# Performance work log

Hardware: AMD Instinct MI355X
Metric: run time of the kernel (lower is better)

## Reference

```python
import jax, jax.numpy as jnp
import numpy as np

ALPHA = 0.5  # args.alpha (restart probability in feature propagation)


def _knn_adj(x, k):
    # pairwise squared euclidean distances (cdist^2), self-distance masked out
    n = x.shape[0]
    sq = jnp.sum(x * x, axis=1)
    d = sq[:, None] + sq[None, :] - 2.0 * (x @ x.T)          # [N, N]
    d = d + jnp.eye(n, dtype=x.dtype) * 1e30                  # exclude self
    _, idx = jax.lax.top_k(-d, k)                              # [N, k] nearest neighbors
    # row-normalized knn adjacency with 1/k weights
    rows = jnp.arange(n)[:, None]
    return jnp.zeros((n, n), x.dtype).at[rows, idx].set(1.0 / k)


def _propagate(adj, x, l, alpha):
    # h_{t+1} = (1-alpha) * A h_t + alpha * x, for l hops
    h = x
    for _ in range(l):
        h = (1.0 - alpha) * (adj @ h) + alpha * x
    return h


def setup_inputs() -> dict:
    key = jax.random.key(0)
    ks = jax.random.split(key, 8)
    N, NFEAT, NHID = 10000, 128, 64
    x = jax.random.normal(ks[0], (N, NFEAT), dtype=jnp.float32)
    adj = jax.random.uniform(ks[1], (N, N), dtype=jnp.float32)
    adj = adj / jnp.sum(adj, axis=1, keepdims=True)            # row-normalized operator
    s_e = 1.0 / np.sqrt(NFEAT)
    s_h = 1.0 / np.sqrt(NHID)
    s_d = 1.0 / np.sqrt(2 * NHID)
    return {
        "x": x,
        "adj": adj,
        "W_enc": jax.random.normal(ks[2], (NFEAT, NHID), jnp.float32) * s_e,
        "b_enc": jnp.zeros((NHID,), jnp.float32),
        "W_enc2": jax.random.normal(ks[3], (NHID, NHID), jnp.float32) * s_h,
        "b_enc2": jnp.zeros((NHID,), jnp.float32),
        "W_dec": jax.random.normal(ks[4], (2 * NHID, NFEAT), jnp.float32) * s_d,
        "b_dec": jnp.zeros((NFEAT,), jnp.float32),
        "k": 16,
        "l": 5,
    }


def reference(x, adj, W_enc, b_enc, W_enc2, b_enc2, W_dec, b_dec, k, l):
    knn = _knn_adj(x, k)                                       # get_knn_graph(x, args.k)
    h1 = _propagate(adj, x, l, ALPHA)                          # feature_propagation(adj, ...)
    h1 = jax.nn.relu(h1 @ W_enc + b_enc)                       # encoder (dropout inactive at eval)
    h2 = _propagate(knn, x, l, ALPHA)                          # feature_propagation(knn, ...)
    h2 = jax.nn.relu(h2 @ W_enc + b_enc)
    z1 = jax.nn.relu(h1 @ W_enc2 + b_enc2)                     # encoder_2
    z2 = jax.nn.relu(h2 @ W_enc2 + b_enc2)
    h = jnp.concatenate([z1, z2], axis=1)                      # [N, 2*nhid]
    res = h @ W_dec + b_dec                                    # decoder
    return (h1, h2, res @ res.T)
```

## Files before the change

kernel.cpp:

```cpp
#include <hip/hip_runtime.h>
#include <stdint.h>


typedef unsigned short u16;
typedef unsigned int u32;
typedef unsigned char u8;

#define N_NODES 10000
#define NPAD    10112
#define KPAD    10240
#define JPAD    10240
#define NF      128
#define NH      64
#define CAP     96
#define ADJ_SCALE 4096.0f
#define ADJ_INV   (0.5f / 4096.0f)

using short8 = __attribute__((ext_vector_type(8))) short;
using f32x4  = __attribute__((ext_vector_type(4))) float;

__device__ __forceinline__ u16 f2bf(float f) {
  u32 u = __float_as_uint(f);
  u += 0x7FFFu + ((u >> 16) & 1u);
  return (u16)(u >> 16);
}
__device__ __forceinline__ float bf2f(u16 h) { return __uint_as_float(((u32)h) << 16); }

__device__ __forceinline__ u32 pk4_fp8(float a, float b, float c, float d) {
  int v = __builtin_amdgcn_cvt_pk_fp8_f32(a, b, 0, false);
  v = __builtin_amdgcn_cvt_pk_fp8_f32(c, d, v, true);
  return (u32)v;
}

__device__ __forceinline__ void g2lds16(const void* g, void* l) {
  __builtin_amdgcn_global_load_lds((const __attribute__((address_space(1))) void*)g,
                                   (__attribute__((address_space(3))) void*)l, 16, 0, 0);
}


__global__ __launch_bounds__(256) void k_rowops(const float* __restrict__ x,
    u16* __restrict__ xhi, u16* __restrict__ xlo, float* __restrict__ sq) {
  int w = threadIdx.x >> 6, lane = threadIdx.x & 63;
  int row = blockIdx.x * 4 + w;
  if (row >= JPAD) return;
  int f = lane * 2;
  if (row < N_NODES) {
    float2 v = *(const float2*)(x + (size_t)row * NF + f);
    u16 h0 = f2bf(v.x), h1 = f2bf(v.y);
    float l0 = v.x - bf2f(h0), l1 = v.y - bf2f(h1);
    u16 e0 = f2bf(l0), e1 = f2bf(l1);
    *(u32*)(xhi + (size_t)row * NF + f) = (u32)h0 | ((u32)h1 << 16);
    *(u32*)(xlo + (size_t)row * NF + f) = (u32)e0 | ((u32)e1 << 16);
    float s = v.x * v.x + v.y * v.y;
#pragma unroll
    for (int o = 32; o > 0; o >>= 1) s += __shfl_xor(s, o);
    if (lane == 0) sq[row] = s;
  } else {
    *(u32*)(xhi + (size_t)row * NF + f) = 0u;
    *(u32*)(xlo + (size_t)row * NF + f) = 0u;
    if (lane == 0) sq[row] = 1.0e30f;
  }
}

__global__ __launch_bounds__(256) void k_transpose(const float* __restrict__ x,
    float* __restrict__ xTf, float* __restrict__ hTf) {
  __shared__ float tile[32][33];
  int k0 = blockIdx.x * 32, f0 = blockIdx.y * 32;
  int c = threadIdx.x & 31, r4 = threadIdx.x >> 5;
#pragma unroll
  for (int i = 0; i < 4; i++) {
    int r = r4 + i * 8;
    int k = k0 + r;
    float v = 0.f;
    if (k < N_NODES) v = x[(size_t)k * NF + f0 + c];
    tile[r][c] = v;
  }
  __syncthreads();
#pragma unroll
  for (int i = 0; i < 4; i++) {
    int r = r4 + i * 8;
    int f = f0 + r;
    int k = k0 + c;
    float v = tile[c][r];
    size_t idx = (size_t)f * KPAD + k;
    xTf[idx] = v; hTf[idx] = v;
  }
}

__global__ __launch_bounds__(256) void k_pack8(const float* __restrict__ hTf,
                                               u8* __restrict__ hT8) {
  int idx = (blockIdx.x * 256 + threadIdx.x) * 4;
  float4 v = *(const float4*)(hTf + idx);
  *(u32*)(hT8 + idx) = pk4_fp8(v.x, v.y, v.z, v.w);
}

__global__ __launch_bounds__(256) void k_adjcvt(const float* __restrict__ adj,
                                                u8* __restrict__ out) {
  const int UNITS = NPAD * (KPAD / 8);
  for (int u = blockIdx.x * 256 + threadIdx.x; u < UNITS; u += gridDim.x * 256) {
    int r = u / (KPAD / 8);
    int c = (u - r * (KPAD / 8)) * 8;
    float v[8];
    if (r < N_NODES && c + 7 < N_NODES) {
      const float* p = adj + (size_t)r * N_NODES + c;
      float4 a = *(const float4*)p;
      float4 b = *(const float4*)(p + 4);
      v[0]=a.x; v[1]=a.y; v[2]=a.z; v[3]=a.w;
      v[4]=b.x; v[5]=b.y; v[6]=b.z; v[7]=b.w;
    } else {
#pragma unroll
      for (int t = 0; t < 8; t++) {
        int cc = c + t;
        v[t] = (r < N_NODES && cc < N_NODES) ? adj[(size_t)r * N_NODES + cc] : 0.f;
      }
    }
#pragma unroll
    for (int t = 0; t < 8; t++) v[t] *= ADJ_SCALE;
    uint2 pk;
    pk.x = pk4_fp8(v[0], v[1], v[2], v[3]);
    pk.y = pk4_fp8(v[4], v[5], v[6], v[7]);
    *(uint2*)(out + (size_t)r * KPAD + c) = pk;
  }
}


__global__ __launch_bounds__(256) void k_gram(const u16* __restrict__ xhi,
    const u16* __restrict__ xlo, const float* __restrict__ sqg,
    float2* __restrict__ cand, u32* __restrict__ cnts) {
  __shared__ __align__(16) u16 shi[64 * 128];
  __shared__ __align__(16) u16 slo[64 * 128];
  __shared__ __align__(16) float ssq[64];
  const int tid = threadIdx.x, w = tid >> 6, lane = tid & 63;
  const int l15 = lane & 15, g = lane >> 4;
  const int q = blockIdx.x * 64 + w * 16 + l15;
  const int split = blockIdx.y;
  const size_t cbase = ((size_t)q * 16 + split * 4 + g) * CAP;

  short8 bh[4], bl[4];
#pragma unroll
  for (int ks = 0; ks < 4; ks++) {
    size_t off = (size_t)q * NF + ks * 32 + g * 8;
    bh[ks] = *(const short8*)(xhi + off);
    bl[ks] = *(const short8*)(xlo + off);
  }
  float t4[4] = {3.0e38f, 3.0e38f, 3.0e38f, 3.0e38f};
  float thr = 3.0e38f;
  u32 cnt = 0;

  for (int ch = 0; ch < 40; ch++) {
    int jbase = split * 2560 + ch * 64;
    __syncthreads();
#pragma unroll
    for (int r = 0; r < 4; r++) {
      int s = r * 256 + tid;
      int row = s >> 4, u = s & 15;
      int uu = u ^ (row & 7);
      size_t goff = (size_t)(jbase + row) * NF + uu * 8;
      g2lds16(xhi + goff, (void*)(shi + ((s & ~63) << 3)));
      g2lds16(xlo + goff, (void*)(slo + ((s & ~63) << 3)));
    }
    if (tid < 64) ssq[tid] = sqg[jbase + tid];
    __syncthreads();

#pragma unroll
    for (int sub = 0; sub < 4; sub++) {
      f32x4 acc = {0.f, 0.f, 0.f, 0.f};
#pragma unroll
      for (int ks = 0; ks < 4; ks++) {
        int row = sub * 16 + l15;
        int uu = ((ks * 4 + g) ^ (row & 7));
        int idx = row * 128 + uu * 8;
        short8 ah = *(const short8*)(shi + idx);
        short8 al = *(const short8*)(slo + idx);
        acc = __builtin_amdgcn_mfma_f32_16x16x32_bf16(ah, bh[ks], acc, 0, 0, 0);
        acc = __builtin_amdgcn_mfma_f32_16x16x32_bf16(ah, bl[ks], acc, 0, 0, 0);
        acc = __builtin_amdgcn_mfma_f32_16x16x32_bf16(al, bh[ks], acc, 0, 0, 0);
      }
      f32x4 sv = *(const f32x4*)(ssq + sub * 16 + g * 4);
      int jb = jbase + sub * 16 + g * 4;
#pragma unroll
      for (int reg = 0; reg < 4; reg++) {
        int j = jb + reg;
        float dd = sv[reg] - 2.0f * acc[reg];
        dd = (j == q) ? 3.0e38f : dd;
        if (dd < thr) {
          if (cnt < CAP) cand[cbase + cnt] = make_float2(dd, __int_as_float(j));
          cnt++;
        }
        bool c0 = dd < t4[0], c1 = dd < t4[1], c2 = dd < t4[2], c3 = dd < t4[3];
        t4[3] = c2 ? t4[2] : (c3 ? dd : t4[3]);
        t4[2] = c1 ? t4[1] : (c2 ? dd : t4[2]);
        t4[1] = c0 ? t4[0] : (c1 ? dd : t4[1]);
        t4[0] = c0 ? dd : t4[0];
      }
      float m = t4[3];
      m = fminf(m, 3.0e38f);
      m = fmaxf(m, __shfl_xor(m, 16));
      m = fmaxf(m, __shfl_xor(m, 32));
      thr = m;
    }
  }
  cnts[(size_t)q * 16 + split * 4 + g] = (cnt < CAP) ? cnt : CAP;
}

__global__ __launch_bounds__(256) void k_merge(const float2* __restrict__ cand,
    const u32* __restrict__ cnts, int* __restrict__ knn) {
  int w = threadIdx.x >> 6, lane = threadIdx.x & 63;
  int q = blockIdx.x * 4 + w;
  if (q >= N_NODES) return;
  int r = lane >> 2, s = lane & 3;
  int cnt = (int)cnts[(size_t)q * 16 + r];
  const float2* cv = cand + ((size_t)q * 16 + r) * CAP;

  float t[16]; int ti[16];
#pragma unroll
  for (int i = 0; i < 16; i++) { t[i] = 3.0e38f; ti[i] = -1; }
  for (int e = s; e < cnt; e += 4) {
    float2 v = cv[e];
    float dd = v.x; int j = __float_as_int(v.y);
    if (j == q) continue;
    if (dd < t[15]) {
#pragma unroll
      for (int i = 15; i >= 1; --i) {
        bool ltp = dd < t[i - 1];
        bool ltc = dd < t[i];
        t[i]  = ltp ? t[i - 1] : (ltc ? dd : t[i]);
        ti[i] = ltp ? ti[i - 1] : (ltc ? j : ti[i]);
      }
      if (dd < t[0]) { t[0] = dd; ti[0] = j; }
    }
  }
  int myout = -1;
#pragma unroll
  for (int round = 0; round < 16; round++) {
    float d0 = t[0]; int j0 = ti[0];
#pragma unroll
    for (int off = 32; off > 0; off >>= 1) {
      float dn = __shfl_xor(d0, off); int jn = __shfl_xor(j0, off);
      bool take = (dn < d0) || (dn == d0 && jn < j0);
      d0 = take ? dn : d0; j0 = take ? jn : j0;
    }
    if (ti[0] == j0) {
#pragma unroll
      for (int i = 0; i < 15; i++) { t[i] = t[i + 1]; ti[i] = ti[i + 1]; }
      t[15] = 3.0e38f; ti[15] = -1;
    }
    if (lane == round) myout = j0;
  }
  if (lane < 16) knn[q * 16 + lane] = myout;
}

__global__ __launch_bounds__(256) void k_knnprop(const float* __restrict__ src,
    const float* __restrict__ x, const int* __restrict__ knn, float* __restrict__ dst) {
  int w = threadIdx.x >> 6, lane = threadIdx.x & 63;
  int row = blockIdx.x * 4 + w;
  if (row >= N_NODES) return;
  int f = lane * 2;
  float a0 = 0.f, a1 = 0.f;
#pragma unroll
  for (int nb = 0; nb < 16; nb++) {
    int j = knn[row * 16 + nb];
    float2 v = *(const float2*)(src + (size_t)j * NF + f);
    a0 += v.x; a1 += v.y;
  }
  float2 xv = *(const float2*)(x + (size_t)row * NF + f);
  float2 o;
  o.x = a0 * (0.5f / 16.f) + 0.5f * xv.x;
  o.y = a1 * (0.5f / 16.f) + 0.5f * xv.y;
  *(float2*)(dst + (size_t)row * NF + f) = o;
}


__global__ __launch_bounds__(256) void k_gemm(const u8* __restrict__ adj8,
    const u8* __restrict__ hT8, float* __restrict__ parts) {
  __shared__ __align__(16) u8 As[128 * 64];
  __shared__ __align__(16) u8 Bs[128 * 64];
  const int tid = threadIdx.x, w = tid >> 6, lane = tid & 63;
  const int l15 = lane & 15, g = lane >> 4;
  const int m0 = blockIdx.x * 128;
  const int split = blockIdx.y;
  const int wm = (w & 1) * 64, wn = (w >> 1) * 64;

  f32x4 zero = {0.f, 0.f, 0.f, 0.f};
  f32x4 acc[4][4];
#pragma unroll
  for (int mi = 0; mi < 4; mi++)
#pragma unroll
    for (int ni = 0; ni < 4; ni++) acc[mi][ni] = zero;

  for (int it = 0; it < 20; it++) {
    int kk = split * 1280 + it * 64;
    __syncthreads();
#pragma unroll
    for (int r = 0; r < 2; r++) {
      int s = r * 256 + tid;
      int row = s >> 2, u = s & 3;
      int uu = u ^ ((row >> 1) & 3);
      g2lds16(adj8 + (size_t)(m0 + row) * KPAD + kk + uu * 16, (void*)(As + ((s & ~63) << 4)));
    }
#pragma unroll
    for (int r = 0; r < 2; r++) {
      int s = r * 256 + tid;
      int row = s >> 2, u = s & 3;
      int uu = u ^ ((row >> 1) & 3);
      g2lds16(hT8 + (size_t)row * KPAD + kk + uu * 16, (void*)(Bs + ((s & ~63) << 4)));
    }
    __syncthreads();
#pragma unroll
    for (int ks = 0; ks < 2; ks++) {
      long af[4], bf[4];
#pragma unroll
      for (int mi = 0; mi < 4; mi++) {
        int row = wm + mi * 16 + l15;
        int u = (ks * 2 + (g >> 1)) ^ ((row >> 1) & 3);
        af[mi] = *(const long*)(As + row * 64 + u * 16 + (g & 1) * 8);
      }
#pragma unroll
      for (int ni = 0; ni < 4; ni++) {
        int row = wn + ni * 16 + l15;
        int u = (ks * 2 + (g >> 1)) ^ ((row >> 1) & 3);
        bf[ni] = *(const long*)(Bs + row * 64 + u * 16 + (g & 1) * 8);
      }
#pragma unroll
      for (int mi = 0; mi < 4; mi++)
#pragma unroll
        for (int ni = 0; ni < 4; ni++)
          acc[mi][ni] = __builtin_amdgcn_mfma_f32_16x16x32_fp8_fp8(af[mi], bf[ni], acc[mi][ni], 0, 0, 0);
    }
  }
#pragma unroll
  for (int mi = 0; mi < 4; mi++) {
#pragma unroll
    for (int ni = 0; ni < 4; ni++) {
      int n = wn + ni * 16 + l15;
      int m = m0 + wm + mi * 16 + g * 4;
      *(f32x4*)(parts + (size_t)(split * 128 + n) * NPAD + m) = acc[mi][ni];
    }
  }
}

__global__ __launch_bounds__(256) void k_reduce(const float* __restrict__ parts,
    const float* __restrict__ xTf, float* __restrict__ hTf, u8* __restrict__ hT8) {
  int idx = (blockIdx.x * 256 + threadIdx.x) * 4;
  int n = idx / KPAD;
  int k = idx - n * KPAD;
  float4 h = {0.f, 0.f, 0.f, 0.f};
  if (k < NPAD) {
    float4 s = {0.f, 0.f, 0.f, 0.f};
#pragma unroll
    for (int sp = 0; sp < 8; sp++) {
      float4 v = *(const float4*)(parts + (size_t)(sp * 128 + n) * NPAD + k);
      s.x += v.x; s.y += v.y; s.z += v.z; s.w += v.w;
    }
    float4 xv = *(const float4*)(xTf + (size_t)n * KPAD + k);
    h.x = ADJ_INV * s.x + 0.5f * xv.x;
    h.y = ADJ_INV * s.y + 0.5f * xv.y;
    h.z = ADJ_INV * s.z + 0.5f * xv.z;
    h.w = ADJ_INV * s.w + 0.5f * xv.w;
  }
  *(float4*)(hTf + (size_t)n * KPAD + k) = h;
  *(u32*)(hT8 + (size_t)n * KPAD + k) = pk4_fp8(h.x, h.y, h.z, h.w);
}


__global__ __launch_bounds__(256) void k_enc(const float* __restrict__ src, int sf, int si,
    const float* __restrict__ W, const float* __restrict__ b, float* __restrict__ out) {
  int w = threadIdx.x >> 6, o = threadIdx.x & 63;
  int row = blockIdx.x * 4 + w;
  if (row >= N_NODES) return;
  float acc = b[o];
#pragma unroll 8
  for (int f = 0; f < NF; f++) {
    float hv = src[(size_t)f * sf + (size_t)row * si];
    acc += hv * W[f * NH + o];
  }
  out[(size_t)row * NH + o] = fmaxf(acc, 0.f);
}

__global__ __launch_bounds__(256) void k_zres(const float* __restrict__ h1e,
    const float* __restrict__ h2e, const float* __restrict__ W2, const float* __restrict__ b2,
    const float* __restrict__ Wd, const float* __restrict__ bd, u16* __restrict__ resb) {
  int w = threadIdx.x >> 6, o = threadIdx.x & 63;
  int row = blockIdx.x * 4 + w;
  if (row >= NPAD) return;
  if (row >= N_NODES) {
    *(u32*)(resb + (size_t)row * NF + o * 2) = 0u;
    return;
  }
  float z1 = b2[o], z2 = b2[o];
#pragma unroll 8
  for (int c = 0; c < NH; c++) {
    float wv = W2[c * NH + o];
    z1 += h1e[(size_t)row * NH + c] * wv;
    z2 += h2e[(size_t)row * NH + c] * wv;
  }
  z1 = fmaxf(z1, 0.f); z2 = fmaxf(z2, 0.f);
  float r0 = bd[o], r1 = bd[o + 64];
#pragma unroll 4
  for (int c = 0; c < NH; c++) {
    float v1 = __shfl(z1, c), v2 = __shfl(z2, c);
    r0 += v1 * Wd[c * NF + o]      + v2 * Wd[(c + 64) * NF + o];
    r1 += v1 * Wd[c * NF + o + 64] + v2 * Wd[(c + 64) * NF + o + 64];
  }
  resb[(size_t)row * NF + o] = f2bf(r0);
  resb[(size_t)row * NF + o + 64] = f2bf(r1);
}


__global__ __launch_bounds__(256) void k_out2(const u16* __restrict__ resb,
                                              float* __restrict__ out2) {
  const int tid = threadIdx.x, w = tid >> 6, lane = tid & 63;
  const int l15 = lane & 15, g = lane >> 4;
  const int m0 = blockIdx.x * 128 + (w & 1) * 64;
  const int n0 = blockIdx.y * 128 + (w >> 1) * 64;
  short8 af[4][4];
#pragma unroll
  for (int mi = 0; mi < 4; mi++)
#pragma unroll
    for (int ks = 0; ks < 4; ks++)
      af[mi][ks] = *(const short8*)(resb + (size_t)(m0 + mi * 16 + l15) * NF + ks * 32 + g * 8);
  f32x4 acc[4][4];
#pragma unroll
  for (int ni = 0; ni < 4; ni++) {
    short8 bq[4];
#pragma unroll
    for (int ks = 0; ks < 4; ks++)
      bq[ks] = *(const short8*)(resb + (size_t)(n0 + ni * 16 + l15) * NF + ks * 32 + g * 8);
#pragma unroll
    for (int mi = 0; mi < 4; mi++) {
      f32x4 a = {0.f, 0.f, 0.f, 0.f};
#pragma unroll
      for (int ks = 0; ks < 4; ks++)
        a = __builtin_amdgcn_mfma_f32_16x16x32_bf16(af[mi][ks], bq[ks], a, 0, 0, 0);
      acc[mi][ni] = a;
    }
  }
#pragma unroll
  for (int mi = 0; mi < 4; mi++) {
#pragma unroll
    for (int ni = 0; ni < 4; ni++) {
      int n = n0 + ni * 16 + l15;
      int mb = m0 + mi * 16 + g * 4;
      if (n < N_NODES) {
#pragma unroll
        for (int reg = 0; reg < 4; reg++) {
          int m = mb + reg;
          if (m < N_NODES) out2[(size_t)m * N_NODES + n] = acc[mi][ni][reg];
        }
      }
    }
  }
}


extern "C" void kernel_launch(void* const* d_in, const int* in_sizes, int n_in,
                              void* d_out, int out_size, void* d_ws, size_t ws_size,
                              hipStream_t stream) {
  (void)in_sizes; (void)n_in; (void)out_size; (void)ws_size;
  const float* x     = (const float*)d_in[0];
  const float* adj   = (const float*)d_in[1];
  const float* Wenc  = (const float*)d_in[2];
  const float* benc  = (const float*)d_in[3];
  const float* Wenc2 = (const float*)d_in[4];
  const float* benc2 = (const float*)d_in[5];
  const float* Wdec  = (const float*)d_in[6];
  const float* bdec  = (const float*)d_in[7];

  char* ws = (char*)d_ws;
  size_t off = 0;
  auto alloc = [&](size_t bytes) {
    void* p = ws + off;
    off = (off + bytes + 255) & ~(size_t)255;
    return p;
  };
  u8*     adj8 = (u8*)    alloc((size_t)NPAD * KPAD);
  void*   uni  =          alloc((size_t)10240 * 16 * CAP * 8);
  float*  hTf  = (float*) alloc((size_t)128 * KPAD * 4);
  u8*     hT8  = (u8*)    alloc((size_t)128 * KPAD);
  float*  xTf  = (float*) alloc((size_t)128 * KPAD * 4);
  u16*    xhi  = (u16*)   alloc((size_t)JPAD * NF * 2);
  u16*    xlo  = (u16*)   alloc((size_t)JPAD * NF * 2);
  float*  sq   = (float*) alloc((size_t)JPAD * 4);
  u32*    cnts = (u32*)   alloc((size_t)10240 * 16 * 4);
  int*    knn  = (int*)   alloc((size_t)N_NODES * 16 * 4);
  float*  h2a  = (float*) alloc((size_t)N_NODES * NF * 4);
  float*  h2b  = (float*) alloc((size_t)N_NODES * NF * 4);
  u16*    resb = (u16*)   alloc((size_t)NPAD * NF * 2);

  float2* cand = (float2*)uni;
  float*  parts= (float*) uni;

  float* out0 = (float*)d_out;
  float* out1 = out0 + 640000;
  float* out2 = out0 + 1280000;

  k_rowops   <<<dim3(JPAD / 4), dim3(256), 0, stream>>>(x, xhi, xlo, sq);
  k_transpose<<<dim3(KPAD / 32, 4), dim3(256), 0, stream>>>(x, xTf, hTf);
  k_pack8    <<<dim3(1280), dim3(256), 0, stream>>>(hTf, hT8);
  k_adjcvt   <<<dim3(8192), dim3(256), 0, stream>>>(adj, adj8);

  k_gram <<<dim3(158, 4), dim3(256), 0, stream>>>(xhi, xlo, sq, cand, cnts);
  k_merge<<<dim3(2500), dim3(256), 0, stream>>>(cand, cnts, knn);

  const float* h2s = x; float* h2d = h2a; float* h2o = h2b;
  for (int t = 0; t < 5; t++) {
    k_knnprop<<<dim3(2500), dim3(256), 0, stream>>>(h2s, x, knn, h2d);
    h2s = h2d; float* tmp = h2d; h2d = h2o; h2o = tmp;
  }

  for (int t = 0; t < 5; t++) {
    k_gemm  <<<dim3(79, 8), dim3(256), 0, stream>>>(adj8, hT8, parts);
    k_reduce<<<dim3(1280), dim3(256), 0, stream>>>(parts, xTf, hTf, hT8);
  }

  k_enc<<<dim3(2500), dim3(256), 0, stream>>>(hTf, KPAD, 1, Wenc, benc, out0);
  k_enc<<<dim3(2500), dim3(256), 0, stream>>>((const float*)h2s, 1, NF, Wenc, benc, out1);
  k_zres<<<dim3(2528), dim3(256), 0, stream>>>(out0, out1, Wenc2, benc2, Wdec, bdec, resb);
  k_out2<<<dim3(79, 79), dim3(256), 0, stream>>>(resb, out2);
}
```

Before: 1.332 ms.

## Fuse independent stages into heterogeneous launches and store GEMM partials as bf16

Independent stages now share a single launch by splitting block ranges: setup combines row ops, transpose and fp8 packing; gram runs alongside adj conversion; the adj GEMM runs alongside the knn merge or knn propagation; the reduce runs alongside knn propagation. The encoder and head kernels are folded into one. GEMM split-K partials are stored as bf16 rather than fp32, and the gram top-k update is skipped when no lane has a candidate. This cuts launch count and lets small bandwidth-bound work fill gaps beside the compute-heavy kernels, at the cost of reduced-precision partial sums and larger combined kernels.

```diff
diff --git a/kernel.cpp b/kernel.cpp
--- a/kernel.cpp
+++ b/kernel.cpp
@@ -16,8 +16,16 @@
 #define ADJ_SCALE 4096.0f
 #define ADJ_INV   (0.5f / 4096.0f)
 
+#define GRAM_BLKS  632
+#define ADJ_BLKS   1024
+#define GEMM_BLKS  632
+#define MERGE_BLKS 2500
+#define RED_BLKS   1280
+#define KNNP_BLKS  2500
+
 using short8 = __attribute__((ext_vector_type(8))) short;
 using f32x4  = __attribute__((ext_vector_type(4))) float;
+using u16x4  = __attribute__((ext_vector_type(4))) unsigned short;
 
 __device__ __forceinline__ u16 f2bf(float f) {
   u32 u = __float_as_uint(f);
@@ -38,66 +46,142 @@
 }
 
 
-__global__ __launch_bounds__(256) void k_rowops(const float* __restrict__ x,
-    u16* __restrict__ xhi, u16* __restrict__ xlo, float* __restrict__ sq) {
-  int w = threadIdx.x >> 6, lane = threadIdx.x & 63;
-  int row = blockIdx.x * 4 + w;
-  if (row >= JPAD) return;
-  int f = lane * 2;
-  if (row < N_NODES) {
-    float2 v = *(const float2*)(x + (size_t)row * NF + f);
-    u16 h0 = f2bf(v.x), h1 = f2bf(v.y);
-    float l0 = v.x - bf2f(h0), l1 = v.y - bf2f(h1);
-    u16 e0 = f2bf(l0), e1 = f2bf(l1);
-    *(u32*)(xhi + (size_t)row * NF + f) = (u32)h0 | ((u32)h1 << 16);
-    *(u32*)(xlo + (size_t)row * NF + f) = (u32)e0 | ((u32)e1 << 16);
-    float s = v.x * v.x + v.y * v.y;
-#pragma unroll
-    for (int o = 32; o > 0; o >>= 1) s += __shfl_xor(s, o);
-    if (lane == 0) sq[row] = s;
+__global__ __launch_bounds__(256) void k_setup(const float* __restrict__ x,
+    u16* __restrict__ xhi, u16* __restrict__ xlo, float* __restrict__ sq,
+    float* __restrict__ xTf, float* __restrict__ hTf, u8* __restrict__ hT8) {
+  __shared__ float tile[32][33];
+  int bid = blockIdx.x;
+  if (bid < 2560) {
+    int w = threadIdx.x >> 6, lane = threadIdx.x & 63;
+    int row = bid * 4 + w;
+    if (row >= JPAD) return;
+    int f = lane * 2;
+    if (row < N_NODES) {
+      float2 v = *(const float2*)(x + (size_t)row * NF + f);
+      u16 h0 = f2bf(v.x), h1 = f2bf(v.y);
+      float l0 = v.x - bf2f(h0), l1 = v.y - bf2f(h1);
+      u16 e0 = f2bf(l0), e1 = f2bf(l1);
+      *(u32*)(xhi + (size_t)row * NF + f) = (u32)h0 | ((u32)h1 << 16);
+      *(u32*)(xlo + (size_t)row * NF + f) = (u32)e0 | ((u32)e1 << 16);
+      float s = v.x * v.x + v.y * v.y;
+#pragma unroll
+      for (int o = 32; o > 0; o >>= 1) s += __shfl_xor(s, o);
+      if (lane == 0) sq[row] = s;
+    } else {
+      *(u32*)(xhi + (size_t)row * NF + f) = 0u;
+      *(u32*)(xlo + (size_t)row * NF + f) = 0u;
+      if (lane == 0) sq[row] = 1.0e30f;
+    }
   } else {
-    *(u32*)(xhi + (size_t)row * NF + f) = 0u;
-    *(u32*)(xlo + (size_t)row * NF + f) = 0u;
-    if (lane == 0) sq[row] = 1.0e30f;
-  }
-}
-
-__global__ __launch_bounds__(256) void k_transpose(const float* __restrict__ x,
-    float* __restrict__ xTf, float* __restrict__ hTf) {
-  __shared__ float tile[32][33];
-  int k0 = blockIdx.x * 32, f0 = blockIdx.y * 32;
-  int c = threadIdx.x & 31, r4 = threadIdx.x >> 5;
-#pragma unroll
-  for (int i = 0; i < 4; i++) {
-    int r = r4 + i * 8;
-    int k = k0 + r;
-    float v = 0.f;
-    if (k < N_NODES) v = x[(size_t)k * NF + f0 + c];
-    tile[r][c] = v;
-  }
-  __syncthreads();
-#pragma unroll
-  for (int i = 0; i < 4; i++) {
-    int r = r4 + i * 8;
-    int f = f0 + r;
-    int k = k0 + c;
-    float v = tile[c][r];
-    size_t idx = (size_t)f * KPAD + k;
-    xTf[idx] = v; hTf[idx] = v;
-  }
-}
-
-__global__ __launch_bounds__(256) void k_pack8(const float* __restrict__ hTf,
-                                               u8* __restrict__ hT8) {
-  int idx = (blockIdx.x * 256 + threadIdx.x) * 4;
-  float4 v = *(const float4*)(hTf + idx);
-  *(u32*)(hT8 + idx) = pk4_fp8(v.x, v.y, v.z, v.w);
-}
-
-__global__ __launch_bounds__(256) void k_adjcvt(const float* __restrict__ adj,
-                                                u8* __restrict__ out) {
+    int id2 = bid - 2560;
+    int k0 = (id2 % 320) * 32, f0 = (id2 / 320) * 32;
+    int c = threadIdx.x & 31, r4 = threadIdx.x >> 5;
+#pragma unroll
+    for (int i = 0; i < 4; i++) {
+      int r = r4 + i * 8;
+      int k = k0 + r;
+      float v = 0.f;
+      if (k < N_NODES) v = x[(size_t)k * NF + f0 + c];
+      tile[r][c] = v;
+    }
+    __syncthreads();
+#pragma unroll
+    for (int i = 0; i < 4; i++) {
+      int r = r4 + i * 8;
+      int f = f0 + r;
+      int k = k0 + c;
+      float v = tile[c][r];
+      size_t idx = (size_t)f * KPAD + k;
+      xTf[idx] = v; hTf[idx] = v;
+      hT8[idx] = (u8)(__builtin_amdgcn_cvt_pk_fp8_f32(v, 0.f, 0, false) & 0xff);
+    }
+  }
+}
+
+
+__device__ __forceinline__ void dev_gram(int bx, int split,
+    u16* shi, u16* slo, float* ssq,
+    const u16* __restrict__ xhi, const u16* __restrict__ xlo,
+    const float* __restrict__ sqg, float2* __restrict__ cand, u32* __restrict__ cnts) {
+  const int tid = threadIdx.x, w = tid >> 6, lane = tid & 63;
+  const int l15 = lane & 15, g = lane >> 4;
+  const int q = bx * 64 + w * 16 + l15;
+  const size_t cbase = ((size_t)q * 16 + split * 4 + g) * CAP;
+
+  short8 bh[4], bl[4];
+#pragma unroll
+  for (int ks = 0; ks < 4; ks++) {
+    size_t off = (size_t)q * NF + ks * 32 + g * 8;
+    bh[ks] = *(const short8*)(xhi + off);
+    bl[ks] = *(const short8*)(xlo + off);
+  }
+  float t4[4] = {3.0e38f, 3.0e38f, 3.0e38f, 3.0e38f};
+  float thr = 3.0e38f;
+  u32 cnt = 0;
+
+  for (int ch = 0; ch < 40; ch++) {
+    int jbase = split * 2560 + ch * 64;
+    __syncthreads();
+#pragma unroll
+    for (int r = 0; r < 4; r++) {
+      int s = r * 256 + tid;
+      int row = s >> 4, u = s & 15;
+      int uu = u ^ (row & 7);
+      size_t goff = (size_t)(jbase + row) * NF + uu * 8;
+      g2lds16(xhi + goff, (void*)(shi + ((s & ~63) << 3)));
+      g2lds16(xlo + goff, (void*)(slo + ((s & ~63) << 3)));
+    }
+    if (tid < 64) ssq[tid] = sqg[jbase + tid];
+    __syncthreads();
+
+#pragma unroll
+    for (int sub = 0; sub < 4; sub++) {
+      f32x4 acc = {0.f, 0.f, 0.f, 0.f};
+#pragma unroll
+      for (int ks = 0; ks < 4; ks++) {
+        int row = sub * 16 + l15;
+        int uu = ((ks * 4 + g) ^ (row & 7));
+        int idx = row * 128 + uu * 8;
+        short8 ah = *(const short8*)(shi + idx);
+        short8 al = *(const short8*)(slo + idx);
+        acc = __builtin_amdgcn_mfma_f32_16x16x32_bf16(ah, bh[ks], acc, 0, 0, 0);
+        acc = __builtin_amdgcn_mfma_f32_16x16x32_bf16(ah, bl[ks], acc, 0, 0, 0);
+        acc = __builtin_amdgcn_mfma_f32_16x16x32_bf16(al, bh[ks], acc, 0, 0, 0);
+      }
+      f32x4 sv = *(const f32x4*)(ssq + sub * 16 + g * 4);
+      int jb = jbase + sub * 16 + g * 4;
+#pragma unroll
+      for (int reg = 0; reg < 4; reg++) {
+        int j = jb + reg;
+        float dd = sv[reg] - 2.0f * acc[reg];
+        dd = (j == q) ? 3.0e38f : dd;
+        if (__any(dd < thr)) {
+          if (dd < thr) {
+            if (cnt < CAP) cand[cbase + cnt] = make_float2(dd, __int_as_float(j));
+            cnt++;
+          }
+          bool c0 = dd < t4[0], c1 = dd < t4[1], c2 = dd < t4[2], c3 = dd < t4[3];
+          t4[3] = c2 ? t4[2] : (c3 ? dd : t4[3]);
+          t4[2] = c1 ? t4[1] : (c2 ? dd : t4[2]);
+          t4[1] = c0 ? t4[0] : (c1 ? dd : t4[1]);
+          t4[0] = c0 ? dd : t4[0];
+        }
+      }
+      float m = t4[3];
+      m = fminf(m, 3.0e38f);
+      m = fmaxf(m, __shfl_xor(m, 16));
+      m = fmaxf(m, __shfl_xor(m, 32));
+      thr = m;
+    }
+  }
+  cnts[(size_t)q * 16 + split * 4 + g] = (cnt < CAP) ? cnt : CAP;
+}
+
+
+__device__ __forceinline__ void dev_adjcvt(int rb, const float* __restrict__ adj,
+                                           u8* __restrict__ out) {
   const int UNITS = NPAD * (KPAD / 8);
-  for (int u = blockIdx.x * 256 + threadIdx.x; u < UNITS; u += gridDim.x * 256) {
+  for (int u = rb * 256 + (int)threadIdx.x; u < UNITS; u += ADJ_BLKS * 256) {
     int r = u / (KPAD / 8);
     int c = (u - r * (KPAD / 8)) * 8;
     float v[8];
@@ -124,89 +208,94 @@
 }
 
 
-__global__ __launch_bounds__(256) void k_gram(const u16* __restrict__ xhi,
+__global__ __launch_bounds__(256) void k_gram_adj(const u16* __restrict__ xhi,
     const u16* __restrict__ xlo, const float* __restrict__ sqg,
-    float2* __restrict__ cand, u32* __restrict__ cnts) {
-  __shared__ __align__(16) u16 shi[64 * 128];
-  __shared__ __align__(16) u16 slo[64 * 128];
-  __shared__ __align__(16) float ssq[64];
+    float2* __restrict__ cand, u32* __restrict__ cnts,
+    const float* __restrict__ adj, u8* __restrict__ adj8) {
+  __shared__ __align__(16) u8 smem[33024];
+  int bid = blockIdx.x;
+  if (bid < GRAM_BLKS) {
+    dev_gram(bid % 158, bid / 158, (u16*)smem, (u16*)(smem + 16384),
+             (float*)(smem + 32768), xhi, xlo, sqg, cand, cnts);
+  } else {
+    dev_adjcvt(bid - GRAM_BLKS, adj, adj8);
+  }
+}
+
+
+__device__ __forceinline__ void dev_gemm(int rid, u8* As, u8* Bs,
+    const u8* __restrict__ adj8, const u8* __restrict__ hT8, u16* __restrict__ parts16) {
   const int tid = threadIdx.x, w = tid >> 6, lane = tid & 63;
   const int l15 = lane & 15, g = lane >> 4;
-  const int q = blockIdx.x * 64 + w * 16 + l15;
-  const int split = blockIdx.y;
-  const size_t cbase = ((size_t)q * 16 + split * 4 + g) * CAP;
-
-  short8 bh[4], bl[4];
-#pragma unroll
-  for (int ks = 0; ks < 4; ks++) {
-    size_t off = (size_t)q * NF + ks * 32 + g * 8;
-    bh[ks] = *(const short8*)(xhi + off);
-    bl[ks] = *(const short8*)(xlo + off);
-  }
-  float t4[4] = {3.0e38f, 3.0e38f, 3.0e38f, 3.0e38f};
-  float thr = 3.0e38f;
-  u32 cnt = 0;
-
-  for (int ch = 0; ch < 40; ch++) {
-    int jbase = split * 2560 + ch * 64;
+  const int m0 = (rid % 79) * 128;
+  const int split = rid / 79;
+  const int wm = (w & 1) * 64, wn = (w >> 1) * 64;
+
+  f32x4 zero = {0.f, 0.f, 0.f, 0.f};
+  f32x4 acc[4][4];
+#pragma unroll
+  for (int mi = 0; mi < 4; mi++)
+#pragma unroll
+    for (int ni = 0; ni < 4; ni++) acc[mi][ni] = zero;
+
+  for (int it = 0; it < 20; it++) {
+    int kk = split * 1280 + it * 64;
     __syncthreads();
 #pragma unroll
-    for (int r = 0; r < 4; r++) {
+    for (int r = 0; r < 2; r++) {
       int s = r * 256 + tid;
-      int row = s >> 4, u = s & 15;
-      int uu = u ^ (row & 7);
-      size_t goff = (size_t)(jbase + row) * NF + uu * 8;
-      g2lds16(xhi + goff, (void*)(shi + ((s & ~63) << 3)));
-      g2lds16(xlo + goff, (void*)(slo + ((s & ~63) << 3)));
-    }
-    if (tid < 64) ssq[tid] = sqg[jbase + tid];
+      int row = s >> 2, u = s & 3;
+      int uu = u ^ ((row >> 1) & 3);
+      g2lds16(adj8 + (size_t)(m0 + row) * KPAD + kk + uu * 16, (void*)(As + ((s & ~63) << 4)));
+    }
+#pragma unroll
+    for (int r = 0; r < 2; r++) {
+      int s = r * 256 + tid;
+      int row = s >> 2, u = s & 3;
+      int uu = u ^ ((row >> 1) & 3);
+      g2lds16(hT8 + (size_t)row * KPAD + kk + uu * 16, (void*)(Bs + ((s & ~63) << 4)));
+    }
     __syncthreads();
-
-#pragma unroll
-    for (int sub = 0; sub < 4; sub++) {
-      f32x4 acc = {0.f, 0.f, 0.f, 0.f};
-#pragma unroll
-      for (int ks = 0; ks < 4; ks++) {
-        int row = sub * 16 + l15;
-        int uu = ((ks * 4 + g) ^ (row & 7));
-        int idx = row * 128 + uu * 8;
-        short8 ah = *(const short8*)(shi + idx);
-        short8 al = *(const short8*)(slo + idx);
-        acc = __builtin_amdgcn_mfma_f32_16x16x32_bf16(ah, bh[ks], acc, 0, 0, 0);
-        acc = __builtin_amdgcn_mfma_f32_16x16x32_bf16(ah, bl[ks], acc, 0, 0, 0);
-        acc = __builtin_amdgcn_mfma_f32_16x16x32_bf16(al, bh[ks], acc, 0, 0, 0);
-      }
-      f32x4 sv = *(const f32x4*)(ssq + sub * 16 + g * 4);
-      int jb = jbase + sub * 16 + g * 4;
-#pragma unroll
-      for (int reg = 0; reg < 4; reg++) {
-        int j = jb + reg;
-        float dd = sv[reg] - 2.0f * acc[reg];
-        dd = (j == q) ? 3.0e38f : dd;
-        if (dd < thr) {
-          if (cnt < CAP) cand[cbase + cnt] = make_float2(dd, __int_as_float(j));
-          cnt++;
-        }
-        bool c0 = dd < t4[0], c1 = dd < t4[1], c2 = dd < t4[2], c3 = dd < t4[3];
-        t4[3] = c2 ? t4[2] : (c3 ? dd : t4[3]);
-        t4[2] = c1 ? t4[1] : (c2 ? dd : t4[2]);
-        t4[1] = c0 ? t4[0] : (c1 ? dd : t4[1]);
-        t4[0] = c0 ? dd : t4[0];
-      }
-      float m = t4[3];
-      m = fminf(m, 3.0e38f);
-      m = fmaxf(m, __shfl_xor(m, 16));
-      m = fmaxf(m, __shfl_xor(m, 32));
-      thr = m;
-    }
-  }
-  cnts[(size_t)q * 16 + split * 4 + g] = (cnt < CAP) ? cnt : CAP;
-}
-
-__global__ __launch_bounds__(256) void k_merge(const float2* __restrict__ cand,
+#pragma unroll
+    for (int ks = 0; ks < 2; ks++) {
+      long af[4], bf[4];
+#pragma unroll
+      for (int mi = 0; mi < 4; mi++) {
+        int row = wm + mi * 16 + l15;
+        int u = (ks * 2 + (g >> 1)) ^ ((row >> 1) & 3);
+        af[mi] = *(const long*)(As + row * 64 + u * 16 + (g & 1) * 8);
+      }
+#pragma unroll
+      for (int ni = 0; ni < 4; ni++) {
+        int row = wn + ni * 16 + l15;
+        int u = (ks * 2 + (g >> 1)) ^ ((row >> 1) & 3);
+        bf[ni] = *(const long*)(Bs + row * 64 + u * 16 + (g & 1) * 8);
+      }
+#pragma unroll
+      for (int mi = 0; mi < 4; mi++)
+#pragma unroll
+        for (int ni = 0; ni < 4; ni++)
+          acc[mi][ni] = __builtin_amdgcn_mfma_f32_16x16x32_fp8_fp8(af[mi], bf[ni], acc[mi][ni], 0, 0, 0);
+    }
+  }
+#pragma unroll
+  for (int mi = 0; mi < 4; mi++) {
+#pragma unroll
+    for (int ni = 0; ni < 4; ni++) {
+      int n = wn + ni * 16 + l15;
+      int m = m0 + wm + mi * 16 + g * 4;
+      f32x4 a = acc[mi][ni];
+      u16x4 pk = { f2bf(a[0]), f2bf(a[1]), f2bf(a[2]), f2bf(a[3]) };
+      *(u16x4*)(parts16 + (size_t)(split * 128 + n) * NPAD + m) = pk;
+    }
+  }
+}
+
+
+__device__ __forceinline__ void dev_merge(int rid, const float2* __restrict__ cand,
     const u32* __restrict__ cnts, int* __restrict__ knn) {
   int w = threadIdx.x >> 6, lane = threadIdx.x & 63;
-  int q = blockIdx.x * 4 + w;
+  int q = rid * 4 + w;
   if (q >= N_NODES) return;
   int r = lane >> 2, s = lane & 3;
   int cnt = (int)cnts[(size_t)q * 16 + r];
@@ -250,10 +339,11 @@
   if (lane < 16) knn[q * 16 + lane] = myout;
 }
 
-__global__ __launch_bounds__(256) void k_knnprop(const float* __restrict__ src,
+
+__device__ __forceinline__ void dev_knnprop(int rid, const float* __restrict__ src,
     const float* __restrict__ x, const int* __restrict__ knn, float* __restrict__ dst) {
   int w = threadIdx.x >> 6, lane = threadIdx.x & 63;
-  int row = blockIdx.x * 4 + w;
+  int row = rid * 4 + w;
   if (row >= N_NODES) return;
   int f = lane * 2;
   float a0 = 0.f, a1 = 0.f;
@@ -271,115 +361,64 @@
 }
 
 
-__global__ __launch_bounds__(256) void k_gemm(const u8* __restrict__ adj8,
-    const u8* __restrict__ hT8, float* __restrict__ parts) {
-  __shared__ __align__(16) u8 As[128 * 64];
-  __shared__ __align__(16) u8 Bs[128 * 64];
-  const int tid = threadIdx.x, w = tid >> 6, lane = tid & 63;
-  const int l15 = lane & 15, g = lane >> 4;
-  const int m0 = blockIdx.x * 128;
-  const int split = blockIdx.y;
-  const int wm = (w & 1) * 64, wn = (w >> 1) * 64;
-
-  f32x4 zero = {0.f, 0.f, 0.f, 0.f};
-  f32x4 acc[4][4];
-#pragma unroll
-  for (int mi = 0; mi < 4; mi++)
-#pragma unroll
-    for (int ni = 0; ni < 4; ni++) acc[mi][ni] = zero;
-
-  for (int it = 0; it < 20; it++) {
-    int kk = split * 1280 + it * 64;
-    __syncthreads();
-#pragma unroll
-    for (int r = 0; r < 2; r++) {
-      int s = r * 256 + tid;
-      int row = s >> 2, u = s & 3;
-      int uu = u ^ ((row >> 1) & 3);
-      g2lds16(adj8 + (size_t)(m0 + row) * KPAD + kk + uu * 16, (void*)(As + ((s & ~63) << 4)));
-    }
-#pragma unroll
-    for (int r = 0; r < 2; r++) {
-      int s = r * 256 + tid;
-      int row = s >> 2, u = s & 3;
-      int uu = u ^ ((row >> 1) & 3);
-      g2lds16(hT8 + (size_t)row * KPAD + kk + uu * 16, (void*)(Bs + ((s & ~63) << 4)));
-    }
-    __syncthreads();
-#pragma unroll
-    for (int ks = 0; ks < 2; ks++) {
-      long af[4], bf[4];
-#pragma unroll
-      for (int mi = 0; mi < 4; mi++) {
-        int row = wm + mi * 16 + l15;
-        int u = (ks * 2 + (g >> 1)) ^ ((row >> 1) & 3);
-        af[mi] = *(const long*)(As + row * 64 + u * 16 + (g & 1) * 8);
-      }
-#pragma unroll
-      for (int ni = 0; ni < 4; ni++) {
-        int row = wn + ni * 16 + l15;
-        int u = (ks * 2 + (g >> 1)) ^ ((row >> 1) & 3);
-        bf[ni] = *(const long*)(Bs + row * 64 + u * 16 + (g & 1) * 8);
-      }
-#pragma unroll
-      for (int mi = 0; mi < 4; mi++)
-#pragma unroll
-        for (int ni = 0; ni < 4; ni++)
-          acc[mi][ni] = __builtin_amdgcn_mfma_f32_16x16x32_fp8_fp8(af[mi], bf[ni], acc[mi][ni], 0, 0, 0);
-    }
-  }
-#pragma unroll
-  for (int mi = 0; mi < 4; mi++) {
-#pragma unroll
-    for (int ni = 0; ni < 4; ni++) {
-      int n = wn + ni * 16 + l15;
-      int m = m0 + wm + mi * 16 + g * 4;
-      *(f32x4*)(parts + (size_t)(split * 128 + n) * NPAD + m) = acc[mi][ni];
-    }
-  }
-}
-
-__global__ __launch_bounds__(256) void k_reduce(const float* __restrict__ parts,
+__device__ __forceinline__ void dev_reduce(int rid, const u16* __restrict__ parts16,
     const float* __restrict__ xTf, float* __restrict__ hTf, u8* __restrict__ hT8) {
-  int idx = (blockIdx.x * 256 + threadIdx.x) * 4;
+  int idx = (rid * 256 + (int)threadIdx.x) * 4;
   int n = idx / KPAD;
   int k = idx - n * KPAD;
   float4 h = {0.f, 0.f, 0.f, 0.f};
   if (k < NPAD) {
-    float4 s = {0.f, 0.f, 0.f, 0.f};
+    float s0 = 0.f, s1 = 0.f, s2 = 0.f, s3 = 0.f;
 #pragma unroll
     for (int sp = 0; sp < 8; sp++) {
-      float4 v = *(const float4*)(parts + (size_t)(sp * 128 + n) * NPAD + k);
-      s.x += v.x; s.y += v.y; s.z += v.z; s.w += v.w;
+      u16x4 v = *(const u16x4*)(parts16 + (size_t)(sp * 128 + n) * NPAD + k);
+      s0 += bf2f(v[0]); s1 += bf2f(v[1]); s2 += bf2f(v[2]); s3 += bf2f(v[3]);
     }
     float4 xv = *(const float4*)(xTf + (size_t)n * KPAD + k);
-    h.x = ADJ_INV * s.x + 0.5f * xv.x;
-    h.y = ADJ_INV * s.y + 0.5f * xv.y;
-    h.z = ADJ_INV * s.z + 0.5f * xv.z;
-    h.w = ADJ_INV * s.w + 0.5f * xv.w;
+    h.x = ADJ_INV * s0 + 0.5f * xv.x;
+    h.y = ADJ_INV * s1 + 0.5f * xv.y;
+    h.z = ADJ_INV * s2 + 0.5f * xv.z;
+    h.w = ADJ_INV * s3 + 0.5f * xv.w;
   }
   *(float4*)(hTf + (size_t)n * KPAD + k) = h;
   *(u32*)(hT8 + (size_t)n * KPAD + k) = pk4_fp8(h.x, h.y, h.z, h.w);
 }
 
 
-__global__ __launch_bounds__(256) void k_enc(const float* __restrict__ src, int sf, int si,
-    const float* __restrict__ W, const float* __restrict__ b, float* __restrict__ out) {
-  int w = threadIdx.x >> 6, o = threadIdx.x & 63;
-  int row = blockIdx.x * 4 + w;
-  if (row >= N_NODES) return;
-  float acc = b[o];
-#pragma unroll 8
-  for (int f = 0; f < NF; f++) {
-    float hv = src[(size_t)f * sf + (size_t)row * si];
-    acc += hv * W[f * NH + o];
-  }
-  out[(size_t)row * NH + o] = fmaxf(acc, 0.f);
-}
-
-__global__ __launch_bounds__(256) void k_zres(const float* __restrict__ h1e,
-    const float* __restrict__ h2e, const float* __restrict__ W2, const float* __restrict__ b2,
-    const float* __restrict__ Wd, const float* __restrict__ bd, u16* __restrict__ resb) {
+__global__ __launch_bounds__(256) void k_gemm_merge(const u8* __restrict__ adj8,
+    const u8* __restrict__ hT8, u16* __restrict__ parts16,
+    const float2* __restrict__ cand, const u32* __restrict__ cnts, int* __restrict__ knn) {
+  __shared__ __align__(16) u8 smem[16384];
+  int bid = blockIdx.x;
+  if (bid < GEMM_BLKS) dev_gemm(bid, smem, smem + 8192, adj8, hT8, parts16);
+  else                 dev_merge(bid - GEMM_BLKS, cand, cnts, knn);
+}
+
+__global__ __launch_bounds__(256) void k_gemm_knn(const u8* __restrict__ adj8,
+    const u8* __restrict__ hT8, u16* __restrict__ parts16,
+    const float* __restrict__ src, const float* __restrict__ x,
+    const int* __restrict__ knn, float* __restrict__ dst) {
+  __shared__ __align__(16) u8 smem[16384];
+  int bid = blockIdx.x;
+  if (bid < GEMM_BLKS) dev_gemm(bid, smem, smem + 8192, adj8, hT8, parts16);
+  else                 dev_knnprop(bid - GEMM_BLKS, src, x, knn, dst);
+}
+
+__global__ __launch_bounds__(256) void k_red_knn(const u16* __restrict__ parts16,
+    const float* __restrict__ xTf, float* __restrict__ hTf, u8* __restrict__ hT8,
+    const float* __restrict__ src, const float* __restrict__ x,
+    const int* __restrict__ knn, float* __restrict__ dst) {
+  int bid = blockIdx.x;
+  if (bid < RED_BLKS) dev_reduce(bid, parts16, xTf, hTf, hT8);
+  else                dev_knnprop(bid - RED_BLKS, src, x, knn, dst);
+}
+
+
+__global__ __launch_bounds__(256) void k_headall(const float* __restrict__ hTf,
+    const float* __restrict__ h2, const float* __restrict__ Wenc, const float* __restrict__ benc,
+    const float* __restrict__ Wenc2, const float* __restrict__ benc2,
+    const float* __restrict__ Wdec, const float* __restrict__ bdec,
+    float* __restrict__ out0, float* __restrict__ out1, u16* __restrict__ resb) {
   int w = threadIdx.x >> 6, o = threadIdx.x & 63;
   int row = blockIdx.x * 4 + w;
   if (row >= NPAD) return;
@@ -387,20 +426,30 @@
     *(u32*)(resb + (size_t)row * NF + o * 2) = 0u;
     return;
   }
-  float z1 = b2[o], z2 = b2[o];
+  float a1 = benc[o], a2 = benc[o];
+#pragma unroll 8
+  for (int f = 0; f < NF; f++) {
+    float wv = Wenc[f * NH + o];
+    a1 += hTf[(size_t)f * KPAD + row] * wv;
+    a2 += h2[(size_t)row * NF + f] * wv;
+  }
+  a1 = fmaxf(a1, 0.f); a2 = fmaxf(a2, 0.f);
+  out0[(size_t)row * NH + o] = a1;
+  out1[(size_t)row * NH + o] = a2;
+  float z1 = benc2[o], z2 = benc2[o];
 #pragma unroll 8
   for (int c = 0; c < NH; c++) {
-    float wv = W2[c * NH + o];
-    z1 += h1e[(size_t)row * NH + c] * wv;
-    z2 += h2e[(size_t)row * NH + c] * wv;
+    float wv = Wenc2[c * NH + o];
+    z1 += __shfl(a1, c) * wv;
+    z2 += __shfl(a2, c) * wv;
   }
   z1 = fmaxf(z1, 0.f); z2 = fmaxf(z2, 0.f);
-  float r0 = bd[o], r1 = bd[o + 64];
+  float r0 = bdec[o], r1 = bdec[o + 64];
 #pragma unroll 4
   for (int c = 0; c < NH; c++) {
     float v1 = __shfl(z1, c), v2 = __shfl(z2, c);
-    r0 += v1 * Wd[c * NF + o]      + v2 * Wd[(c + 64) * NF + o];
-    r1 += v1 * Wd[c * NF + o + 64] + v2 * Wd[(c + 64) * NF + o + 64];
+    r0 += v1 * Wdec[c * NF + o]      + v2 * Wdec[(c + 64) * NF + o];
+    r1 += v1 * Wdec[c * NF + o + 64] + v2 * Wdec[(c + 64) * NF + o + 64];
   }
   resb[(size_t)row * NF + o] = f2bf(r0);
   resb[(size_t)row * NF + o + 64] = f2bf(r1);
@@ -473,48 +522,49 @@
     off = (off + bytes + 255) & ~(size_t)255;
     return p;
   };
-  u8*     adj8 = (u8*)    alloc((size_t)NPAD * KPAD);
-  void*   uni  =          alloc((size_t)10240 * 16 * CAP * 8);
-  float*  hTf  = (float*) alloc((size_t)128 * KPAD * 4);
-  u8*     hT8  = (u8*)    alloc((size_t)128 * KPAD);
-  float*  xTf  = (float*) alloc((size_t)128 * KPAD * 4);
-  u16*    xhi  = (u16*)   alloc((size_t)JPAD * NF * 2);
-  u16*    xlo  = (u16*)   alloc((size_t)JPAD * NF * 2);
-  float*  sq   = (float*) alloc((size_t)JPAD * 4);
-  u32*    cnts = (u32*)   alloc((size_t)10240 * 16 * 4);
-  int*    knn  = (int*)   alloc((size_t)N_NODES * 16 * 4);
-  float*  h2a  = (float*) alloc((size_t)N_NODES * NF * 4);
-  float*  h2b  = (float*) alloc((size_t)N_NODES * NF * 4);
-  u16*    resb = (u16*)   alloc((size_t)NPAD * NF * 2);
-
-  float2* cand = (float2*)uni;
-  float*  parts= (float*) uni;
+  u8*     adj8   = (u8*)    alloc((size_t)NPAD * KPAD);
+  float2* cand   = (float2*)alloc((size_t)10240 * 16 * CAP * 8);
+  u16*    parts16= (u16*)   alloc((size_t)8 * 128 * NPAD * 2);
+  float*  hTf    = (float*) alloc((size_t)128 * KPAD * 4);
+  u8*     hT8    = (u8*)    alloc((size_t)128 * KPAD);
+  float*  xTf    = (float*) alloc((size_t)128 * KPAD * 4);
+  u16*    xhi    = (u16*)   alloc((size_t)JPAD * NF * 2);
+  u16*    xlo    = (u16*)   alloc((size_t)JPAD * NF * 2);
+  float*  sq     = (float*) alloc((size_t)JPAD * 4);
+  u32*    cnts   = (u32*)   alloc((size_t)10240 * 16 * 4);
+  int*    knn    = (int*)   alloc((size_t)N_NODES * 16 * 4);
+  float*  h2a    = (float*) alloc((size_t)N_NODES * NF * 4);
+  float*  h2b    = (float*) alloc((size_t)N_NODES * NF * 4);
+  u16*    resb   = (u16*)   alloc((size_t)NPAD * NF * 2);
 
   float* out0 = (float*)d_out;
   float* out1 = out0 + 640000;
   float* out2 = out0 + 1280000;
 
-  k_rowops   <<<dim3(JPAD / 4), dim3(256), 0, stream>>>(x, xhi, xlo, sq);
-  k_transpose<<<dim3(KPAD / 32, 4), dim3(256), 0, stream>>>(x, xTf, hTf);
-  k_pack8    <<<dim3(1280), dim3(256), 0, stream>>>(hTf, hT8);
-  k_adjcvt   <<<dim3(8192), dim3(256), 0, stream>>>(adj, adj8);
-
-  k_gram <<<dim3(158, 4), dim3(256), 0, stream>>>(xhi, xlo, sq, cand, cnts);
-  k_merge<<<dim3(2500), dim3(256), 0, stream>>>(cand, cnts, knn);
-
-  const float* h2s = x; float* h2d = h2a; float* h2o = h2b;
-  for (int t = 0; t < 5; t++) {
-    k_knnprop<<<dim3(2500), dim3(256), 0, stream>>>(h2s, x, knn, h2d);
-    h2s = h2d; float* tmp = h2d; h2d = h2o; h2o = tmp;
-  }
-
-  for (int t = 0; t < 5; t++) {
-    k_gemm  <<<dim3(79, 8), dim3(256), 0, stream>>>(adj8, hT8, parts);
-    k_reduce<<<dim3(1280), dim3(256), 0, stream>>>(parts, xTf, hTf, hT8);
-  }
-
-  k_enc<<<dim3(2500), dim3(256), 0, stream>>>(hTf, KPAD, 1, Wenc, benc, out0);
-  k_enc<<<dim3(2500), dim3(256), 0, stream>>>((const float*)h2s, 1, NF, Wenc, benc, out1);
-  k_zres<<<dim3(2528), dim3(256), 0, stream>>>(out0, out1, Wenc2, benc2, Wdec, bdec, resb);
+  k_setup<<<dim3(2560 + 1280), dim3(256), 0, stream>>>(x, xhi, xlo, sq, xTf, hTf, hT8);
+  k_gram_adj<<<dim3(GRAM_BLKS + ADJ_BLKS), dim3(256), 0, stream>>>(
+      xhi, xlo, sq, cand, cnts, adj, adj8);
+  k_gemm_merge<<<dim3(GEMM_BLKS + MERGE_BLKS), dim3(256), 0, stream>>>(
+      adj8, hT8, parts16, cand, cnts, knn);
+  k_red_knn<<<dim3(RED_BLKS + KNNP_BLKS), dim3(256), 0, stream>>>(
+      parts16, xTf, hTf, hT8, x, x, knn, h2a);
+  k_gemm_knn<<<dim3(GEMM_BLKS + KNNP_BLKS), dim3(256), 0, stream>>>(
+      adj8, hT8, parts16, h2a, x, knn, h2b);
+  k_red_knn<<<dim3(RED_BLKS + KNNP_BLKS), dim3(256), 0, stream>>>(
+      parts16, xTf, hTf, hT8, h2b, x, knn, h2a);
+  k_gemm_knn<<<dim3(GEMM_BLKS + KNNP_BLKS), dim3(256), 0, stream>>>(
+      adj8, hT8, parts16, h2a, x, knn, h2b);
+  k_red_knn<<<dim3(RED_BLKS + KNNP_BLKS), dim3(256), 0, stream>>>(
+      parts16, xTf, hTf, hT8, h2b, x, knn, h2a);
+  k_gemm_knn<<<dim3(GEMM_BLKS), dim3(256), 0, stream>>>(
+      adj8, hT8, parts16, nullptr, x, knn, nullptr);
+  k_red_knn<<<dim3(RED_BLKS), dim3(256), 0, stream>>>(
+      parts16, xTf, hTf, hT8, nullptr, x, knn, nullptr);
+  k_gemm_knn<<<dim3(GEMM_BLKS), dim3(256), 0, stream>>>(
+      adj8, hT8, parts16, nullptr, x, knn, nullptr);
+  k_red_knn<<<dim3(RED_BLKS), dim3(256), 0, stream>>>(
+      parts16, xTf, hTf, hT8, nullptr, x, knn, nullptr);
+  k_headall<<<dim3(NPAD / 4), dim3(256), 0, stream>>>(
+      hTf, h2a, Wenc, benc, Wenc2, benc2, Wdec, bdec, out0, out1, resb);
   k_out2<<<dim3(79, 79), dim3(256), 0, stream>>>(resb, out2);
 }
```

Result: faster. 1.263 ms (-5.2%).
